# Kernel optimization log

Hardware: AMD Instinct MI355X
Metric: run time of the kernel (lower is better)

Reference implementation:

```python
import jax, jax.numpy as jnp
import numpy as np

DIM = 32
BATCH = 131072
NH = 100

def _init_linear(key, nin, nout):
    k1, k2 = jax.random.split(key)
    bound = 1.0 / np.sqrt(nin)
    W = jax.random.uniform(k1, (nin, nout), minval=-bound, maxval=bound, dtype=jnp.float32)
    b = jax.random.uniform(k2, (nout,), minval=-bound, maxval=bound, dtype=jnp.float32)
    return W, b

def setup_inputs() -> dict:
    key = jax.random.key(0)
    ks = jax.random.split(key, 8)
    e = jax.random.normal(ks[0], (BATCH, DIM), dtype=jnp.float32)
    # causal adjacency: strictly upper-triangular random 0/1 (parents j of node i satisfy j < i)
    Craw = jax.random.bernoulli(ks[1], 0.5, (DIM, DIM)).astype(jnp.float32)
    C = Craw * jnp.triu(jnp.ones((DIM, DIM), jnp.float32), k=1)
    s_W1, s_b1 = _init_linear(ks[2], DIM, NH)
    s_W2, s_b2 = _init_linear(ks[3], NH, NH)
    s_W3, s_b3 = _init_linear(ks[4], NH, 1)
    t_W1, t_b1 = _init_linear(ks[5], DIM, NH)
    t_W2, t_b2 = _init_linear(ks[6], NH, NH)
    t_W3, t_b3 = _init_linear(ks[7], NH, 1)
    return {"e": e, "C": C,
            "s_W1": s_W1, "s_b1": s_b1, "s_W2": s_W2, "s_b2": s_b2, "s_W3": s_W3, "s_b3": s_b3,
            "t_W1": t_W1, "t_b1": t_b1, "t_W2": t_W2, "t_b2": t_b2, "t_W3": t_W3, "t_b3": t_b3}

def _mlp(x, W1, b1, W2, b2, W3, b3):
    # linear -> relu -> linear -> relu -> linear -> sigmoid, squeeze last dim
    h = jax.nn.relu(x @ W1 + b1)
    h = jax.nn.relu(h @ W2 + b2)
    return jax.nn.sigmoid(h @ W3 + b3)[:, 0]  # [B]

def reference(e, C, s_W1, s_b1, s_W2, s_b2, s_W3, s_b3, t_W1, t_b1, t_W2, t_b2, t_W3, t_b3):
    B, dim = e.shape

    def step(carry, xs):
        z, log_det = carry
        i, mask, e_i = xs          # mask = C[:, i] (all-zero column == zero mask branch in torch)
        x = z * mask               # [B, dim]
        s = _mlp(x, s_W1, s_b1, s_W2, s_b2, s_W3, s_b3)
        t = _mlp(x, t_W1, t_b1, t_W2, t_b2, t_W3, t_b3)
        z = z.at[:, i].set(jnp.exp(s) * e_i + t)
        return (z, log_det + s), None

    init = (jnp.zeros_like(e), jnp.zeros((B,), e.dtype))
    (z, log_det), _ = jax.lax.scan(step, init, (jnp.arange(dim), C.T, e.T))
    return z, log_det
```

## Files before the change

kernel.cpp:

```cpp
#include <hip/hip_runtime.h>


typedef __attribute__((ext_vector_type(8))) short short8;
typedef __attribute__((ext_vector_type(4))) float f32x4;
typedef __attribute__((ext_vector_type(16))) float f32x16;
typedef __attribute__((ext_vector_type(4))) unsigned int uint4v;

#define WPK_U16 44032
#define MPK_OFF_BYTES 88064
#define NBLK 1024
#define REPS 4

__device__ __forceinline__ unsigned int bf16u(float v) {
  unsigned int b = __float_as_uint(v);
  b += 0x7FFFu + ((b >> 16) & 1u);
  return b >> 16;
}

__device__ __forceinline__ unsigned int cvtpk(float lo, float hi) {
  unsigned int r;
  asm("v_cvt_pk_bf16_f32 %0, %1, %2" : "=v"(r) : "v"(lo), "v"(hi));
  return r;
}

__device__ __forceinline__ unsigned int pkrelu(unsigned int x) {
  unsigned int r;
  asm("v_pk_max_i16 %0, %1, %2" : "=v"(r) : "v"(x), "v"(0u));
  return r;
}

__device__ __forceinline__ short8 packBC(const f32x16 &ht, int c) {
  uint4v u;
  u.x = pkrelu(cvtpk(ht[c * 8 + 0], ht[c * 8 + 1]));
  u.y = pkrelu(cvtpk(ht[c * 8 + 2], ht[c * 8 + 3]));
  u.z = pkrelu(cvtpk(ht[c * 8 + 4], ht[c * 8 + 5]));
  u.w = pkrelu(cvtpk(ht[c * 8 + 6], ht[c * 8 + 7]));
  return __builtin_bit_cast(short8, u);
}

__device__ __forceinline__ short8 packBC6(const f32x16 &ht, bool bh) {
  uint4v u;
  float lo = bh ? 1.0f : ht[0];
  u.x = pkrelu(cvtpk(lo, ht[1]));
  u.y = pkrelu(cvtpk(ht[2], ht[3]));
  u.z = pkrelu(cvtpk(ht[4], ht[5]));
  u.w = pkrelu(cvtpk(ht[6], ht[7]));
  return __builtin_bit_cast(short8, u);
}

__device__ __forceinline__ float mlp32(const short8 (&a1)[4][2],
                                       const short8 (&a2)[4][7],
                                       const short8 *__restrict__ a3,
                                       short8 x0, short8 x1, bool bh) {
  const f32x16 zz = {0.f, 0.f, 0.f, 0.f, 0.f, 0.f, 0.f, 0.f,
                     0.f, 0.f, 0.f, 0.f, 0.f, 0.f, 0.f, 0.f};
  f32x16 h1[4];
#pragma unroll
  for (int T = 0; T < 4; ++T)
    h1[T] = __builtin_amdgcn_mfma_f32_32x32x16_bf16(a1[T][0], x0, zz, 0, 0, 0);
#pragma unroll
  for (int T = 0; T < 4; ++T)
    h1[T] = __builtin_amdgcn_mfma_f32_32x32x16_bf16(a1[T][1], x1, h1[T], 0, 0, 0);

  short8 bf0 = packBC(h1[0], 0), bf1 = packBC(h1[0], 1);
  short8 bf2 = packBC(h1[1], 0), bf3 = packBC(h1[1], 1);
  short8 bf4 = packBC(h1[2], 0), bf5 = packBC(h1[2], 1);
  short8 bf6 = packBC6(h1[3], bh);

  f32x16 h2[4];
#pragma unroll
  for (int M = 0; M < 4; ++M)
    h2[M] = __builtin_amdgcn_mfma_f32_32x32x16_bf16(a2[M][0], bf0, zz, 0, 0, 0);
#pragma unroll
  for (int M = 0; M < 4; ++M)
    h2[M] = __builtin_amdgcn_mfma_f32_32x32x16_bf16(a2[M][1], bf1, h2[M], 0, 0, 0);
#pragma unroll
  for (int M = 0; M < 4; ++M)
    h2[M] = __builtin_amdgcn_mfma_f32_32x32x16_bf16(a2[M][2], bf2, h2[M], 0, 0, 0);
#pragma unroll
  for (int M = 0; M < 4; ++M)
    h2[M] = __builtin_amdgcn_mfma_f32_32x32x16_bf16(a2[M][3], bf3, h2[M], 0, 0, 0);
#pragma unroll
  for (int M = 0; M < 4; ++M)
    h2[M] = __builtin_amdgcn_mfma_f32_32x32x16_bf16(a2[M][4], bf4, h2[M], 0, 0, 0);
#pragma unroll
  for (int M = 0; M < 4; ++M)
    h2[M] = __builtin_amdgcn_mfma_f32_32x32x16_bf16(a2[M][5], bf5, h2[M], 0, 0, 0);
#pragma unroll
  for (int M = 0; M < 4; ++M)
    h2[M] = __builtin_amdgcn_mfma_f32_32x32x16_bf16(a2[M][6], bf6, h2[M], 0, 0, 0);

  short8 bg0 = packBC(h2[0], 0), bg1 = packBC(h2[0], 1);
  short8 bg2 = packBC(h2[1], 0), bg3 = packBC(h2[1], 1);
  short8 bg4 = packBC(h2[2], 0), bg5 = packBC(h2[2], 1);
  short8 bg6 = packBC6(h2[3], bh);

  f32x16 acc0 = __builtin_amdgcn_mfma_f32_32x32x16_bf16(a3[0], bg0, zz, 0, 0, 0);
  f32x16 acc1 = __builtin_amdgcn_mfma_f32_32x32x16_bf16(a3[64], bg1, zz, 0, 0, 0);
  acc0 = __builtin_amdgcn_mfma_f32_32x32x16_bf16(a3[128], bg2, acc0, 0, 0, 0);
  acc1 = __builtin_amdgcn_mfma_f32_32x32x16_bf16(a3[192], bg3, acc1, 0, 0, 0);
  acc0 = __builtin_amdgcn_mfma_f32_32x32x16_bf16(a3[256], bg4, acc0, 0, 0, 0);
  acc1 = __builtin_amdgcn_mfma_f32_32x32x16_bf16(a3[320], bg5, acc1, 0, 0, 0);
  acc0 = __builtin_amdgcn_mfma_f32_32x32x16_bf16(a3[384], bg6, acc0, 0, 0, 0);
  return acc0[0] + acc1[0];
}

__global__ void prepack_kernel(const float *__restrict__ C,
                               const float *__restrict__ sW1, const float *__restrict__ sb1,
                               const float *__restrict__ sW2, const float *__restrict__ sb2,
                               const float *__restrict__ sW3, const float *__restrict__ sb3,
                               const float *__restrict__ tW1, const float *__restrict__ tb1,
                               const float *__restrict__ tW2, const float *__restrict__ tb2,
                               const float *__restrict__ tW3, const float *__restrict__ tb3,
                               unsigned short *__restrict__ wpk,
                               unsigned int *__restrict__ mpk) {
  int gid = blockIdx.x * 256 + threadIdx.x;
  if (gid < WPK_U16) {
    int which = gid / 22016;
    int a = gid % 22016;
    const float *W1 = which ? tW1 : sW1;
    const float *B1 = which ? tb1 : sb1;
    const float *W2 = which ? tW2 : sW2;
    const float *B2 = which ? tb2 : sb2;
    const float *W3 = which ? tW3 : sW3;
    const float *B3 = which ? tb3 : sb3;
    int f = a >> 9;
    int l = (a >> 3) & 63;
    int j = a & 7;
    int hh = l >> 5, cl = l & 31;
    float v = 0.f;
    if (f < 8) {
      int T = f >> 1, c = f & 1;
      int m = 32 * T + cl;
      int d = 16 * c + 8 * hh + j;
      if (m < 100) v = (d == 31) ? B1[m] : W1[d * 100 + m];
    } else if (f < 36) {
      int ff = f - 8;
      int M = ff / 7, kk = ff % 7;
      int m = 32 * M + cl;
      int q = (kk & 1) * 8 + j;
      int n = 32 * (kk >> 1) + (q & 3) + 8 * (q >> 2) + 4 * hh;
      if (m < 100) {
        if (n < 100) v = W2[n * 100 + m];
        else if (n == 100) v = B2[m];
      }
    } else {
      int kk = f - 36;
      int q = (kk & 1) * 8 + j;
      int n = 32 * (kk >> 1) + (q & 3) + 8 * (q >> 2) + 4 * hh;
      if (n < 100) v = W3[n];
      else if (n == 100) v = B3[0];
    }
    wpk[gid] = (unsigned short)bf16u(v);
  } else if (gid < WPK_U16 + 512) {
    int idx = gid - WPK_U16;
    int i = idx >> 4;
    int hh = (idx >> 3) & 1;
    int p = idx & 7;
    int d0 = 16 * (p >> 2) + 8 * hh + 2 * (p & 3);
    unsigned int u = 0;
    if (C[d0 * 32 + i] != 0.f) u |= 0x0000FFFFu;
    if (C[(d0 + 1) * 32 + i] != 0.f) u |= 0xFFFF0000u;
    mpk[idx] = u;
  }
}

__global__ __launch_bounds__(64, 1) void flow_main(
    const float *__restrict__ e, const unsigned short *__restrict__ wpk,
    const unsigned int *__restrict__ mpk, float *__restrict__ out) {
  const int lane = threadIdx.x;
  const int h = lane >> 5;
  const int col = lane & 31;
  const bool hb = (h == 1);

  __shared__ __align__(16) unsigned int msk[512];
  __shared__ short8 a3l[896];
  {
    const uint4v *s = (const uint4v *)mpk;
    uint4v *d = (uint4v *)msk;
    d[lane] = s[lane];
    d[lane + 64] = s[lane + 64];
  }
  const short8 *wfr = (const short8 *)wpk;
#pragma unroll
  for (int f = 0; f < 14; ++f) {
    int mlp = f / 7, kk = f % 7;
    a3l[f * 64 + lane] = wfr[(mlp * 43 + 36 + kk) * 64 + lane];
  }

  short8 a1s[4][2], a2s[4][7], a1t[4][2], a2t[4][7];
#pragma unroll
  for (int T = 0; T < 4; ++T)
#pragma unroll
    for (int c = 0; c < 2; ++c) {
      a1s[T][c] = wfr[(T * 2 + c) * 64 + lane];
      a1t[T][c] = wfr[(43 + T * 2 + c) * 64 + lane];
    }
#pragma unroll
  for (int M = 0; M < 4; ++M)
#pragma unroll
    for (int k = 0; k < 7; ++k) {
      a2s[M][k] = wfr[(8 + M * 7 + k) * 64 + lane];
      a2t[M][k] = wfr[(43 + 8 + M * 7 + k) * 64 + lane];
    }
#pragma unroll
  for (int M = 0; M < 4; ++M)
#pragma unroll
    for (int k = 0; k < 7; ++k) {
      asm volatile("" : "+a"(a2s[M][k]));
      asm volatile("" : "+a"(a2t[M][k]));
    }
  __syncthreads();

  const short8 *a3s = a3l + lane;
  const short8 *a3t = a3l + 7 * 64 + lane;

#pragma unroll 1
  for (int rep = 0; rep < REPS; ++rep) {
    const long row = ((long)blockIdx.x * REPS + rep) * 32 + col;
    const float *ep = e + row * 32;
    f32x4 eA = *(const f32x4 *)(ep + 8 * h);
    f32x4 eB = *(const f32x4 *)(ep + 8 * h + 4);
    f32x4 eC = *(const f32x4 *)(ep + 16 + 8 * h);
    f32x4 eD = *(const f32x4 *)(ep + 16 + 8 * h + 4);
    unsigned int zr[8] = {0u, 0u, 0u, 0u, 0u, 0u, 0u, 0u};
    float ld = 0.f;
    uint4v ma = *(const uint4v *)&msk[h * 8];
    uint4v mb = *(const uint4v *)&msk[h * 8 + 4];

#pragma unroll 1
    for (int i8 = 0; i8 < 4; ++i8) {
      const bool tg = (h == (i8 & 1));
#pragma unroll
      for (int u = 0; u < 8; ++u) {
        const int nx = (((i8 * 8 + u) + 1) & 31) * 16 + h * 8;
        uint4v man = *(const uint4v *)&msk[nx];
        uint4v mbn = *(const uint4v *)&msk[nx + 4];

        uint4v xu0, xu1;
        xu0.x = zr[0] & ma.x; xu0.y = zr[1] & ma.y;
        xu0.z = zr[2] & ma.z; xu0.w = zr[3] & ma.w;
        xu1.x = zr[4] & mb.x; xu1.y = zr[5] & mb.y;
        xu1.z = zr[6] & mb.z; xu1.w = zr[7] & mb.w;
        if (hb) xu1.w = (xu1.w & 0x0000FFFFu) | 0x3F800000u;
        short8 x0 = __builtin_bit_cast(short8, xu0);
        short8 x1 = __builtin_bit_cast(short8, xu1);

        float sp = mlp32(a1s, a2s, a3s, x0, x1, hb);
        float tp = mlp32(a1t, a2t, a3t, x0, x1, hb);
        float sv = __fdividef(1.f, 1.f + __expf(-sp));
        float tv = __fdividef(1.f, 1.f + __expf(-tp));
        ld += sv;

        float es0 = (u < 4) ? eA[u] : eB[u - 4];
        float es1 = (u < 4) ? eC[u] : eD[u - 4];
        float es = (i8 < 2) ? es0 : es1;
        float zn = __expf(sv) * es + tv;
        unsigned int r = cvtpk(zn, zn);
        const int p = u >> 1;
        const bool hi = (u & 1) != 0;
        if (i8 < 2) {
          unsigned int mrg = hi ? ((zr[p] & 0x0000FFFFu) | (r & 0xFFFF0000u))
                                : ((zr[p] & 0xFFFF0000u) | (r & 0x0000FFFFu));
          zr[p] = tg ? mrg : zr[p];
        } else {
          unsigned int mrg = hi ? ((zr[4 + p] & 0x0000FFFFu) | (r & 0xFFFF0000u))
                                : ((zr[4 + p] & 0xFFFF0000u) | (r & 0x0000FFFFu));
          zr[4 + p] = tg ? mrg : zr[4 + p];
        }
        ma = man;
        mb = mbn;
      }
    }

    float *zo = out + row * 32;
    f32x4 o;
    o[0] = __uint_as_float(zr[0] << 16);
    o[1] = __uint_as_float(zr[0] & 0xFFFF0000u);
    o[2] = __uint_as_float(zr[1] << 16);
    o[3] = __uint_as_float(zr[1] & 0xFFFF0000u);
    *(f32x4 *)(zo + 8 * h) = o;
    o[0] = __uint_as_float(zr[2] << 16);
    o[1] = __uint_as_float(zr[2] & 0xFFFF0000u);
    o[2] = __uint_as_float(zr[3] << 16);
    o[3] = __uint_as_float(zr[3] & 0xFFFF0000u);
    *(f32x4 *)(zo + 8 * h + 4) = o;
    o[0] = __uint_as_float(zr[4] << 16);
    o[1] = __uint_as_float(zr[4] & 0xFFFF0000u);
    o[2] = __uint_as_float(zr[5] << 16);
    o[3] = __uint_as_float(zr[5] & 0xFFFF0000u);
    *(f32x4 *)(zo + 16 + 8 * h) = o;
    o[0] = __uint_as_float(zr[6] << 16);
    o[1] = __uint_as_float(zr[6] & 0xFFFF0000u);
    o[2] = __uint_as_float(zr[7] << 16);
    o[3] = __uint_as_float(zr[7] & 0xFFFF0000u);
    *(f32x4 *)(zo + 16 + 8 * h + 4) = o;
    if (h == 0) out[(long)131072 * 32 + row] = ld;
  }
}

extern "C" void kernel_launch(void *const *d_in, const int *in_sizes, int n_in,
                              void *d_out, int out_size, void *d_ws, size_t ws_size,
                              hipStream_t stream) {
  const float *e  = (const float *)d_in[0];
  const float *C  = (const float *)d_in[1];
  const float *sW1 = (const float *)d_in[2];
  const float *sb1 = (const float *)d_in[3];
  const float *sW2 = (const float *)d_in[4];
  const float *sb2 = (const float *)d_in[5];
  const float *sW3 = (const float *)d_in[6];
  const float *sb3 = (const float *)d_in[7];
  const float *tW1 = (const float *)d_in[8];
  const float *tb1 = (const float *)d_in[9];
  const float *tW2 = (const float *)d_in[10];
  const float *tb2 = (const float *)d_in[11];
  const float *tW3 = (const float *)d_in[12];
  const float *tb3 = (const float *)d_in[13];

  unsigned short *wpk = (unsigned short *)d_ws;
  unsigned int *mpk = (unsigned int *)((char *)d_ws + MPK_OFF_BYTES);
  float *out = (float *)d_out;

  prepack_kernel<<<dim3(174), dim3(256), 0, stream>>>(
      C, sW1, sb1, sW2, sb2, sW3, sb3, tW1, tb1, tW2, tb2, tW3, tb3, wpk, mpk);
  flow_main<<<dim3(NBLK), dim3(64), 0, stream>>>(e, wpk, mpk, out);
}
```

Baseline: 279.8 us.

## Interleave s and t MLP chains and move layer-1 weights to LDS

Merges the two per-step MLP evaluations into one function that interleaves the s and t MFMA chains layer by layer, so each MFMA's dependency latency can be hidden by independent work from the other network. Layer-1 weight fragments move from registers into shared memory to free register/AGPR pressure. The cost is extra LDS reads of the layer-1 weights on every step, and more live accumulators at once from the interleaving.

```diff
diff --git a/kernel.cpp b/kernel.cpp
--- a/kernel.cpp
+++ b/kernel.cpp
@@ -48,61 +48,61 @@
   return __builtin_bit_cast(short8, u);
 }
 
-__device__ __forceinline__ float mlp32(const short8 (&a1)[4][2],
-                                       const short8 (&a2)[4][7],
-                                       const short8 *__restrict__ a3,
-                                       short8 x0, short8 x1, bool bh) {
+__device__ __forceinline__ void mlp2_32(
+    const short8 (&a2s)[4][7], const short8 (&a2t)[4][7],
+    const short8 *__restrict__ a1p, const short8 *__restrict__ a3p,
+    short8 x0, short8 x1, bool bh, float &sp, float &tp) {
   const f32x16 zz = {0.f, 0.f, 0.f, 0.f, 0.f, 0.f, 0.f, 0.f,
                      0.f, 0.f, 0.f, 0.f, 0.f, 0.f, 0.f, 0.f};
-  f32x16 h1[4];
-#pragma unroll
-  for (int T = 0; T < 4; ++T)
-    h1[T] = __builtin_amdgcn_mfma_f32_32x32x16_bf16(a1[T][0], x0, zz, 0, 0, 0);
-#pragma unroll
-  for (int T = 0; T < 4; ++T)
-    h1[T] = __builtin_amdgcn_mfma_f32_32x32x16_bf16(a1[T][1], x1, h1[T], 0, 0, 0);
-
-  short8 bf0 = packBC(h1[0], 0), bf1 = packBC(h1[0], 1);
-  short8 bf2 = packBC(h1[1], 0), bf3 = packBC(h1[1], 1);
-  short8 bf4 = packBC(h1[2], 0), bf5 = packBC(h1[2], 1);
-  short8 bf6 = packBC6(h1[3], bh);
-
-  f32x16 h2[4];
-#pragma unroll
-  for (int M = 0; M < 4; ++M)
-    h2[M] = __builtin_amdgcn_mfma_f32_32x32x16_bf16(a2[M][0], bf0, zz, 0, 0, 0);
-#pragma unroll
-  for (int M = 0; M < 4; ++M)
-    h2[M] = __builtin_amdgcn_mfma_f32_32x32x16_bf16(a2[M][1], bf1, h2[M], 0, 0, 0);
-#pragma unroll
-  for (int M = 0; M < 4; ++M)
-    h2[M] = __builtin_amdgcn_mfma_f32_32x32x16_bf16(a2[M][2], bf2, h2[M], 0, 0, 0);
-#pragma unroll
-  for (int M = 0; M < 4; ++M)
-    h2[M] = __builtin_amdgcn_mfma_f32_32x32x16_bf16(a2[M][3], bf3, h2[M], 0, 0, 0);
-#pragma unroll
-  for (int M = 0; M < 4; ++M)
-    h2[M] = __builtin_amdgcn_mfma_f32_32x32x16_bf16(a2[M][4], bf4, h2[M], 0, 0, 0);
-#pragma unroll
-  for (int M = 0; M < 4; ++M)
-    h2[M] = __builtin_amdgcn_mfma_f32_32x32x16_bf16(a2[M][5], bf5, h2[M], 0, 0, 0);
-#pragma unroll
-  for (int M = 0; M < 4; ++M)
-    h2[M] = __builtin_amdgcn_mfma_f32_32x32x16_bf16(a2[M][6], bf6, h2[M], 0, 0, 0);
-
-  short8 bg0 = packBC(h2[0], 0), bg1 = packBC(h2[0], 1);
-  short8 bg2 = packBC(h2[1], 0), bg3 = packBC(h2[1], 1);
-  short8 bg4 = packBC(h2[2], 0), bg5 = packBC(h2[2], 1);
-  short8 bg6 = packBC6(h2[3], bh);
-
-  f32x16 acc0 = __builtin_amdgcn_mfma_f32_32x32x16_bf16(a3[0], bg0, zz, 0, 0, 0);
-  f32x16 acc1 = __builtin_amdgcn_mfma_f32_32x32x16_bf16(a3[64], bg1, zz, 0, 0, 0);
-  acc0 = __builtin_amdgcn_mfma_f32_32x32x16_bf16(a3[128], bg2, acc0, 0, 0, 0);
-  acc1 = __builtin_amdgcn_mfma_f32_32x32x16_bf16(a3[192], bg3, acc1, 0, 0, 0);
-  acc0 = __builtin_amdgcn_mfma_f32_32x32x16_bf16(a3[256], bg4, acc0, 0, 0, 0);
-  acc1 = __builtin_amdgcn_mfma_f32_32x32x16_bf16(a3[320], bg5, acc1, 0, 0, 0);
-  acc0 = __builtin_amdgcn_mfma_f32_32x32x16_bf16(a3[384], bg6, acc0, 0, 0, 0);
-  return acc0[0] + acc1[0];
+  short8 bfs[7], bft[7];
+#pragma unroll
+  for (int T = 0; T < 4; ++T) {
+    f32x16 hs = __builtin_amdgcn_mfma_f32_32x32x16_bf16(a1p[(T * 2) * 64], x0, zz, 0, 0, 0);
+    f32x16 ht = __builtin_amdgcn_mfma_f32_32x32x16_bf16(a1p[(8 + T * 2) * 64], x0, zz, 0, 0, 0);
+    hs = __builtin_amdgcn_mfma_f32_32x32x16_bf16(a1p[(T * 2 + 1) * 64], x1, hs, 0, 0, 0);
+    ht = __builtin_amdgcn_mfma_f32_32x32x16_bf16(a1p[(8 + T * 2 + 1) * 64], x1, ht, 0, 0, 0);
+    if (T < 3) {
+      bfs[2 * T] = packBC(hs, 0); bfs[2 * T + 1] = packBC(hs, 1);
+      bft[2 * T] = packBC(ht, 0); bft[2 * T + 1] = packBC(ht, 1);
+    } else {
+      bfs[6] = packBC6(hs, bh);
+      bft[6] = packBC6(ht, bh);
+    }
+  }
+  short8 bgs[7], bgt[7];
+#pragma unroll
+  for (int M = 0; M < 4; ++M) {
+    f32x16 hs = __builtin_amdgcn_mfma_f32_32x32x16_bf16(a2s[M][0], bfs[0], zz, 0, 0, 0);
+    f32x16 ht = __builtin_amdgcn_mfma_f32_32x32x16_bf16(a2t[M][0], bft[0], zz, 0, 0, 0);
+#pragma unroll
+    for (int kk = 1; kk < 7; ++kk) {
+      hs = __builtin_amdgcn_mfma_f32_32x32x16_bf16(a2s[M][kk], bfs[kk], hs, 0, 0, 0);
+      ht = __builtin_amdgcn_mfma_f32_32x32x16_bf16(a2t[M][kk], bft[kk], ht, 0, 0, 0);
+    }
+    if (M < 3) {
+      bgs[2 * M] = packBC(hs, 0); bgs[2 * M + 1] = packBC(hs, 1);
+      bgt[2 * M] = packBC(ht, 0); bgt[2 * M + 1] = packBC(ht, 1);
+    } else {
+      bgs[6] = packBC6(hs, bh);
+      bgt[6] = packBC6(ht, bh);
+    }
+  }
+  f32x16 as0 = __builtin_amdgcn_mfma_f32_32x32x16_bf16(a3p[0 * 64], bgs[0], zz, 0, 0, 0);
+  f32x16 at0 = __builtin_amdgcn_mfma_f32_32x32x16_bf16(a3p[7 * 64], bgt[0], zz, 0, 0, 0);
+  f32x16 as1 = __builtin_amdgcn_mfma_f32_32x32x16_bf16(a3p[1 * 64], bgs[1], zz, 0, 0, 0);
+  f32x16 at1 = __builtin_amdgcn_mfma_f32_32x32x16_bf16(a3p[8 * 64], bgt[1], zz, 0, 0, 0);
+  as0 = __builtin_amdgcn_mfma_f32_32x32x16_bf16(a3p[2 * 64], bgs[2], as0, 0, 0, 0);
+  at0 = __builtin_amdgcn_mfma_f32_32x32x16_bf16(a3p[9 * 64], bgt[2], at0, 0, 0, 0);
+  as1 = __builtin_amdgcn_mfma_f32_32x32x16_bf16(a3p[3 * 64], bgs[3], as1, 0, 0, 0);
+  at1 = __builtin_amdgcn_mfma_f32_32x32x16_bf16(a3p[10 * 64], bgt[3], at1, 0, 0, 0);
+  as0 = __builtin_amdgcn_mfma_f32_32x32x16_bf16(a3p[4 * 64], bgs[4], as0, 0, 0, 0);
+  at0 = __builtin_amdgcn_mfma_f32_32x32x16_bf16(a3p[11 * 64], bgt[4], at0, 0, 0, 0);
+  as1 = __builtin_amdgcn_mfma_f32_32x32x16_bf16(a3p[5 * 64], bgs[5], as1, 0, 0, 0);
+  at1 = __builtin_amdgcn_mfma_f32_32x32x16_bf16(a3p[12 * 64], bgt[5], at1, 0, 0, 0);
+  as0 = __builtin_amdgcn_mfma_f32_32x32x16_bf16(a3p[6 * 64], bgs[6], as0, 0, 0, 0);
+  at0 = __builtin_amdgcn_mfma_f32_32x32x16_bf16(a3p[13 * 64], bgt[6], at0, 0, 0, 0);
+  sp = as0[0] + as1[0];
+  tp = at0[0] + at1[0];
 }
 
 __global__ void prepack_kernel(const float *__restrict__ C,
@@ -174,6 +174,7 @@
   const bool hb = (h == 1);
 
   __shared__ __align__(16) unsigned int msk[512];
+  __shared__ short8 a1l[1024];
   __shared__ short8 a3l[896];
   {
     const uint4v *s = (const uint4v *)mpk;
@@ -183,19 +184,17 @@
   }
   const short8 *wfr = (const short8 *)wpk;
 #pragma unroll
+  for (int f = 0; f < 16; ++f) {
+    int mlp = f >> 3, fc = f & 7;
+    a1l[f * 64 + lane] = wfr[(mlp * 43 + fc) * 64 + lane];
+  }
+#pragma unroll
   for (int f = 0; f < 14; ++f) {
     int mlp = f / 7, kk = f % 7;
     a3l[f * 64 + lane] = wfr[(mlp * 43 + 36 + kk) * 64 + lane];
   }
 
-  short8 a1s[4][2], a2s[4][7], a1t[4][2], a2t[4][7];
-#pragma unroll
-  for (int T = 0; T < 4; ++T)
-#pragma unroll
-    for (int c = 0; c < 2; ++c) {
-      a1s[T][c] = wfr[(T * 2 + c) * 64 + lane];
-      a1t[T][c] = wfr[(43 + T * 2 + c) * 64 + lane];
-    }
+  short8 a2s[4][7], a2t[4][7];
 #pragma unroll
   for (int M = 0; M < 4; ++M)
 #pragma unroll
@@ -212,8 +211,8 @@
     }
   __syncthreads();
 
-  const short8 *a3s = a3l + lane;
-  const short8 *a3t = a3l + 7 * 64 + lane;
+  const short8 *a1p = a1l + lane;
+  const short8 *a3p = a3l + lane;
 
 #pragma unroll 1
   for (int rep = 0; rep < REPS; ++rep) {
@@ -246,8 +245,8 @@
         short8 x0 = __builtin_bit_cast(short8, xu0);
         short8 x1 = __builtin_bit_cast(short8, xu1);
 
-        float sp = mlp32(a1s, a2s, a3s, x0, x1, hb);
-        float tp = mlp32(a1t, a2t, a3t, x0, x1, hb);
+        float sp, tp;
+        mlp2_32(a2s, a2t, a1p, a3p, x0, x1, hb, sp, tp);
         float sv = __fdividef(1.f, 1.f + __expf(-sp));
         float tv = __fdividef(1.f, 1.f + __expf(-tp));
         ld += sv;
```

Measured after the change: 438.1 us. +56.6%, slower.
